# Kernel tuning notes

Hardware: AMD Instinct MI355X
Metric: run time of the kernel (lower is better)

## Reference

```python
import jax, jax.numpy as jnp
import numpy as np

N, E, G = 100000, 1600000, 8
IN, H, OUT = 3, 64, 20


def setup_inputs() -> dict:
    key = jax.random.key(0)
    ks = jax.random.split(key, 24)
    def nrm(k, shape, scale=0.1):
        return jax.random.normal(k, shape, dtype=jnp.float32) * scale
    inp = {}
    inp["x"] = jax.random.normal(ks[0], (N, IN), dtype=jnp.float32)
    inp["edge_index"] = jax.random.randint(ks[1], (2, E), 0, N, dtype=jnp.int32)
    inp["batch"] = jnp.sort(jax.random.randint(ks[2], (N,), 0, G, dtype=jnp.int32))
    dims = [(IN, H), (H, H), (H, H)]  # 3 GATConv layers (initial + layers-1)
    for i, (di, do) in enumerate(dims):
        inp[f"W{i}"] = nrm(ks[3 + 4 * i], (di, do))
        inp[f"as{i}"] = nrm(ks[4 + 4 * i], (do,))
        inp[f"ad{i}"] = nrm(ks[5 + 4 * i], (do,))
        inp[f"b{i}"] = jnp.zeros((do,), jnp.float32)
    inp["vn_emb0"] = jnp.zeros((1, H), jnp.float32)  # constant-0 init per module
    inp["m1_w1"] = nrm(ks[15], (H, H)); inp["m1_b1"] = jnp.zeros((H,), jnp.float32)
    inp["m1_w2"] = nrm(ks[16], (H, H)); inp["m1_b2"] = jnp.zeros((H,), jnp.float32)
    inp["mf_w1"] = nrm(ks[17], (H, H)); inp["mf_b1"] = jnp.zeros((H,), jnp.float32)
    inp["mf_w2"] = nrm(ks[18], (H, OUT)); inp["mf_b2"] = jnp.zeros((OUT,), jnp.float32)
    inp["out_w"] = nrm(ks[19], (H, OUT)); inp["out_b"] = jnp.zeros((OUT,), jnp.float32)
    return inp


def _gat(x, src, dst, W, a_s, a_d, b):
    # PyG GATConv, 1 head: h = xW; e_ij = LeakyReLU_0.2(a_s.h_j + a_d.h_i);
    # alpha = softmax over incoming edges of each dst node; out_i = sum_j alpha_ij h_j + b
    h = x @ W                                                  # [N, H]
    lg = jax.nn.leaky_relu((h @ a_s)[src] + (h @ a_d)[dst], 0.2)  # [E+N]
    m = jax.ops.segment_max(lg, dst, num_segments=N)
    m = jnp.where(jnp.isfinite(m), m, 0.0)
    p = jnp.exp(lg - m[dst])
    denom = jax.ops.segment_sum(p, dst, num_segments=N)
    alpha = p / denom[dst]
    return jax.ops.segment_sum(alpha[:, None] * h[src], dst, num_segments=N) + b


def _forward(x, edge_index, batch, params):
    (W0, as0, ad0, b0, W1, as1, ad1, b1, W2, as2, ad2, b2,
     vn_emb0, m1_w1, m1_b1, m1_w2, m1_b2, mf_w1, mf_b1, mf_w2, mf_b2,
     out_w, out_b) = params
    loops = jnp.arange(N, dtype=edge_index.dtype)  # GATConv add_self_loops=True
    src = jnp.concatenate([edge_index[0], loops])
    dst = jnp.concatenate([edge_index[1], loops])
    act = lambda v: jax.nn.leaky_relu(v, 0.01)  # nn.LeakyReLU default slope
    h = act(_gat(x, src, dst, W0, as0, ad0, b0))
    h = act(_gat(h, src, dst, W1, as1, ad1, b1))
    h = act(_gat(h, src, dst, W2, as2, ad2, b2))
    # virtual node: global_add_pool(out, batch) + Embedding(0) (zero-init)
    vn = jax.ops.segment_sum(h, batch, num_segments=G) + vn_emb0[0]
    vn = jax.nn.relu(vn @ m1_w1 + m1_b1)
    vn = jax.nn.relu(vn @ m1_w2 + m1_b2)
    vn = jax.nn.relu(vn @ mf_w1 + mf_b1)
    vn = jax.nn.relu(vn @ mf_w2 + mf_b2)
    return (h @ out_w + out_b, vn)


def reference(x, edge_index, batch, W0, as0, ad0, b0, W1, as1, ad1, b1,
              W2, as2, ad2, b2, vn_emb0, m1_w1, m1_b1, m1_w2, m1_b2,
              mf_w1, mf_b1, mf_w2, mf_b2, out_w, out_b):
    params = (W0, as0, ad0, b0, W1, as1, ad1, b1, W2, as2, ad2, b2,
              vn_emb0, m1_w1, m1_b1, m1_w2, m1_b2, mf_w1, mf_b1, mf_w2, mf_b2,
              out_w, out_b)
    return _forward(x, edge_index, batch, params)
```

## Files before the change

### kernel.cpp

```cpp
#include <hip/hip_runtime.h>
#include <hip/hip_bf16.h>

#define H 64
#define OUTD 20
#define NGRAPH 8
#define NBK 256
#define CAPB 8192
#define MAXDEG 63

typedef __attribute__((ext_vector_type(8))) short bf16x8;
typedef __attribute__((ext_vector_type(4))) float f32x4;
typedef __attribute__((ext_vector_type(8))) unsigned short u16x8;


__device__ __forceinline__ float ldp(const void* p, int i, bool f32) {
    return f32 ? ((const float*)p)[i]
               : __bfloat162float(((const __hip_bfloat16*)p)[i]);
}

__device__ __forceinline__ float bfu(unsigned short u) {
    union { unsigned int i; float f; } c; c.i = ((unsigned)u) << 16; return c.f;
}
__device__ __forceinline__ unsigned short fbits(float f) {
    __hip_bfloat16 b = __float2bfloat16(f);
    return *reinterpret_cast<unsigned short*>(&b);
}

__global__ void detect_dtype(const unsigned short* __restrict__ xb, int n_u16,
                             int* __restrict__ flag) {
    __shared__ int sh[256];
    int t = threadIdx.x;
    int m = min(n_u16, 4096);
    int bad = 0;
    for (int i = t; i < m; i += 256) {
        unsigned e = (xb[i] >> 7) & 0xFF;
        bad += (e >= 0x90) ? 1 : 0;
    }
    sh[t] = bad;
    __syncthreads();
    for (int off = 128; off; off >>= 1) {
        if (t < off) sh[t] += sh[t + off];
        __syncthreads();
    }
    if (t == 0) *flag = (sh[0] > (m >> 4)) ? 1 : 0;
}

__global__ void fillC_dense0(const int* __restrict__ src, const int* __restrict__ dst,
                             int* __restrict__ gcur, unsigned* __restrict__ ebuf,
                             int E, int n, int nC, int EPC, int nbk,
                             const void* __restrict__ x, const void* __restrict__ W,
                             const void* __restrict__ a_s, const void* __restrict__ a_d,
                             __hip_bfloat16* __restrict__ h, float* __restrict__ s,
                             float* __restrict__ d, const int* __restrict__ flagp) {
    if ((int)blockIdx.x < nC) {
        __shared__ unsigned lcnt[NBK];
        __shared__ int lbase[NBK];
        int t = threadIdx.x;
        for (int i = t; i < NBK; i += 256) lcnt[i] = 0;
        __syncthreads();
        int base = blockIdx.x * (256 * EPC) + t;
        for (int i = 0; i < EPC; ++i) {
            int e = base + i * 256;
            if (e < E) {
                int dn = dst[e];
                if ((unsigned)dn < (unsigned)n) atomicAdd(&lcnt[dn >> 9], 1u);
            }
        }
        __syncthreads();
        for (int i = t; i < nbk; i += 256) {
            unsigned c = lcnt[i];
            lbase[i] = c ? atomicAdd(&gcur[i], (int)c) : 0;
            lcnt[i] = 0;
        }
        __syncthreads();
        for (int i = 0; i < EPC; ++i) {
            int e = base + i * 256;
            if (e < E) {
                int dn = dst[e];
                if ((unsigned)dn < (unsigned)n) {
                    int b = dn >> 9;
                    unsigned pos = (unsigned)lbase[b] + atomicAdd(&lcnt[b], 1u);
                    if (pos < CAPB)
                        ebuf[(size_t)b * CAPB + pos] =
                            ((unsigned)src[e] << 9) | (unsigned)(dn & 511);
                }
            }
        }
        return;
    }
    const bool f32 = (*flagp != 0);
    int idx = ((int)blockIdx.x - nC) * 256 + threadIdx.x;
    int node = idx >> 6;
    int f = idx & 63;
    if (node >= n) return;
    float acc = 0.f;
    for (int k = 0; k < 3; ++k)
        acc += ldp(x, node * 3 + k, f32) * ldp(W, k * H + f, f32);
    ((short*)h)[((size_t)(f >> 3) * n + node) * 8 + (f & 7)] = (short)fbits(acc);
    float sv = acc * ldp(a_s, f, f32);
    float dv = acc * ldp(a_d, f, f32);
    for (int off = 32; off; off >>= 1) {
        sv += __shfl_xor(sv, off);
        dv += __shfl_xor(dv, off);
    }
    if (f == 0) { s[node] = sv; d[node] = dv; }
}

__global__ __launch_bounds__(512) void bucketD(const unsigned* __restrict__ ebuf,
                                               const int* __restrict__ gcur,
                                               unsigned* __restrict__ cntoff,
                                               unsigned* __restrict__ col,
                                               int* __restrict__ gtot, int n) {
    __shared__ unsigned lcnt[512];
    __shared__ int loff[512];
    __shared__ int sc[512];
    __shared__ int sdeg[512];
    __shared__ int sbase;
    int b = blockIdx.x, t = threadIdx.x;
    lcnt[t] = 0;
    __syncthreads();
    int end = min(gcur[b], CAPB);
    const unsigned* reg = ebuf + (size_t)b * CAPB;
    for (int i = t; i < end; i += 512) atomicAdd(&lcnt[reg[i] & 511u], 1u);
    __syncthreads();
    int node = (b << 9) + t;
    int degc = (node < n) ? (int)min(lcnt[t], (unsigned)MAXDEG) : -1;
    int slots = degc + 1;
    sc[t] = slots;
    __syncthreads();
    for (int ofs = 1; ofs < 512; ofs <<= 1) {
        int v = (t >= ofs) ? sc[t - ofs] : 0;
        __syncthreads();
        sc[t] += v;
        __syncthreads();
    }
    if (t == 511) sbase = atomicAdd(gtot, sc[511]);
    __syncthreads();
    int myoff = sbase + sc[t] - slots;
    int dg = (degc > 0) ? degc : 0;
    loff[t] = myoff;
    sdeg[t] = dg;
    if (node < n) cntoff[node] = (unsigned)myoff | ((unsigned)dg << 24);
    lcnt[t] = 0;
    __syncthreads();
    for (int i = t; i < end; i += 512) {
        unsigned e = reg[i];
        int loc = (int)(e & 511u);
        unsigned pos = atomicAdd(&lcnt[loc], 1u);
        if ((int)pos < sdeg[loc])
            col[loff[loc] + pos] = (e >> 9) << 15;
    }
}

__global__ void edge_weights(const float* __restrict__ s, const float* __restrict__ d,
                             const unsigned* __restrict__ cntoff,
                             unsigned* __restrict__ col, int n) {
    int node = ((int)blockIdx.x * 256 + (int)threadIdx.x) >> 4;
    if (node >= n) return;
    int l = threadIdx.x & 15;
    unsigned co = cntoff[node];
    int deg = (int)(co >> 24);
    int D = deg + 1;
    unsigned* cb = col + (co & 0xFFFFFFu);
    float di = d[node];
    int dm1 = D - 1;
    int e0 = l, e1 = l + 16, e2 = l + 32, e3 = l + 48;
    unsigned p0 = cb[min(e0, dm1)];
    unsigned p1 = cb[min(e1, dm1)];
    unsigned p2 = cb[min(e2, dm1)];
    unsigned p3 = cb[min(e3, dm1)];
    int j0 = (e0 < deg) ? (int)(p0 >> 15) : node;
    int j1 = (e1 < deg) ? (int)(p1 >> 15) : node;
    int j2 = (e2 < deg) ? (int)(p2 >> 15) : node;
    int j3 = (e3 < deg) ? (int)(p3 >> 15) : node;
    if ((unsigned)j0 >= (unsigned)n) j0 = 0;
    if ((unsigned)j1 >= (unsigned)n) j1 = 0;
    if ((unsigned)j2 >= (unsigned)n) j2 = 0;
    if ((unsigned)j3 >= (unsigned)n) j3 = 0;
    float v0 = s[j0] + di, v1 = s[j1] + di, v2 = s[j2] + di, v3 = s[j3] + di;
    v0 = v0 > 0.f ? v0 : 0.2f * v0;
    v1 = v1 > 0.f ? v1 : 0.2f * v1;
    v2 = v2 > 0.f ? v2 : 0.2f * v2;
    v3 = v3 > 0.f ? v3 : 0.2f * v3;
    bool m0 = e0 < D, m1 = e1 < D, m2 = e2 < D, m3 = e3 < D;
    float a0 = m0 ? v0 : -INFINITY, a1 = m1 ? v1 : -INFINITY;
    float a2 = m2 ? v2 : -INFINITY, a3 = m3 ? v3 : -INFINITY;
    float mx = fmaxf(fmaxf(a0, a1), fmaxf(a2, a3));
    for (int o = 1; o < 16; o <<= 1) mx = fmaxf(mx, __shfl_xor(mx, o));
    float x0 = m0 ? __expf(v0 - mx) : 0.f;
    float x1 = m1 ? __expf(v1 - mx) : 0.f;
    float x2 = m2 ? __expf(v2 - mx) : 0.f;
    float x3 = m3 ? __expf(v3 - mx) : 0.f;
    float ws = x0 + x1 + x2 + x3;
    for (int o = 1; o < 16; o <<= 1) ws += __shfl_xor(ws, o);
    float inv = 1.f / fmaxf(ws, 1e-20f);
    if (m0) cb[e0] = ((unsigned)j0 << 15) |
                     (((__float_as_uint(x0 * inv) + 0x8000u) >> 16) & 0x7FFFu);
    if (m1) cb[e1] = ((unsigned)j1 << 15) |
                     (((__float_as_uint(x1 * inv) + 0x8000u) >> 16) & 0x7FFFu);
    if (m2) cb[e2] = ((unsigned)j2 << 15) |
                     (((__float_as_uint(x2 * inv) + 0x8000u) >> 16) & 0x7FFFu);
    if (m3) cb[e3] = ((unsigned)j3 << 15) |
                     (((__float_as_uint(x3 * inv) + 0x8000u) >> 16) & 0x7FFFu);
}

#define ACC8(w, hv) { \
    a[0] += w * bfu(hv[0]); a[1] += w * bfu(hv[1]); \
    a[2] += w * bfu(hv[2]); a[3] += w * bfu(hv[3]); \
    a[4] += w * bfu(hv[4]); a[5] += w * bfu(hv[5]); \
    a[6] += w * bfu(hv[6]); a[7] += w * bfu(hv[7]); }

__global__ void gat_agg_sliced(const short* __restrict__ hs,
                               const unsigned* __restrict__ cntoff,
                               const unsigned* __restrict__ col,
                               const void* __restrict__ bias,
                               short* __restrict__ outs, int n, int halfN,
                               const int* __restrict__ flagp) {
    const bool f32 = (*flagp != 0);
    int shp = (int)blockIdx.x & 7;
    int sp = shp >> 1, half = shp & 1;
    int node = half * halfN + ((int)blockIdx.x >> 3) * 16 + ((int)threadIdx.x >> 4);
    int lim = half ? n : halfN;
    if (node >= lim) return;
    int l = threadIdx.x & 15;
    int c = l & 1, q = l >> 1;
    unsigned co = cntoff[node];
    int D = (int)(co >> 24) + 1;
    const unsigned* cb = col + (co & 0xFFFFFFu);
    int slice = 2 * sp + c;
    const u16x8* h8 = (const u16x8*)hs + (size_t)slice * n;

    int dm1 = D - 1;
    unsigned pk0 = cb[min(q, dm1)];
    unsigned pk1 = cb[min(q + 8, dm1)];
    unsigned pk2 = cb[min(q + 16, dm1)];
    unsigned pk3 = cb[min(q + 24, dm1)];
    unsigned pk4 = cb[min(q + 32, dm1)];
    unsigned pk5 = cb[min(q + 40, dm1)];
    unsigned pk6 = cb[min(q + 48, dm1)];
    unsigned pk7 = cb[min(q + 56, dm1)];
    pk0 = (q < D) ? pk0 : 0u;
    pk1 = (q + 8 < D) ? pk1 : 0u;
    pk2 = (q + 16 < D) ? pk2 : 0u;
    pk3 = (q + 24 < D) ? pk3 : 0u;
    pk4 = (q + 32 < D) ? pk4 : 0u;
    pk5 = (q + 40 < D) ? pk5 : 0u;
    pk6 = (q + 48 < D) ? pk6 : 0u;
    pk7 = (q + 56 < D) ? pk7 : 0u;

    float a[8] = {0.f, 0.f, 0.f, 0.f, 0.f, 0.f, 0.f, 0.f};
    {
        u16x8 hv0 = h8[pk0 >> 15];
        u16x8 hv1 = h8[pk1 >> 15];
        u16x8 hv2 = h8[pk2 >> 15];
        float w0 = __uint_as_float((pk0 & 0x7FFFu) << 16);
        float w1 = __uint_as_float((pk1 & 0x7FFFu) << 16);
        float w2 = __uint_as_float((pk2 & 0x7FFFu) << 16);
        ACC8(w0, hv0);
        ACC8(w1, hv1);
        ACC8(w2, hv2);
    }
    if (D > 24) {
        u16x8 hv3 = h8[pk3 >> 15];
        u16x8 hv4 = h8[pk4 >> 15];
        u16x8 hv5 = h8[pk5 >> 15];
        u16x8 hv6 = h8[pk6 >> 15];
        u16x8 hv7 = h8[pk7 >> 15];
        float w3 = __uint_as_float((pk3 & 0x7FFFu) << 16);
        float w4 = __uint_as_float((pk4 & 0x7FFFu) << 16);
        float w5 = __uint_as_float((pk5 & 0x7FFFu) << 16);
        float w6 = __uint_as_float((pk6 & 0x7FFFu) << 16);
        float w7 = __uint_as_float((pk7 & 0x7FFFu) << 16);
        ACC8(w3, hv3);
        ACC8(w4, hv4);
        ACC8(w5, hv5);
        ACC8(w6, hv6);
        ACC8(w7, hv7);
    }
#pragma unroll
    for (int i = 0; i < 8; ++i) {
        a[i] += __shfl_xor(a[i], 2);
        a[i] += __shfl_xor(a[i], 4);
        a[i] += __shfl_xor(a[i], 8);
    }
    if (q == 0) {
        u16x8 ov;
        for (int i = 0; i < 8; ++i) {
            float o = a[i] + ldp(bias, slice * 8 + i, f32);
            o = o > 0.f ? o : 0.01f * o;
            ov[i] = fbits(o);
        }
        *((u16x8*)outs + (size_t)slice * n + node) = ov;
    }
}


__global__ __launch_bounds__(256) void denseN_mfma(
    const __hip_bfloat16* __restrict__ in,
    const void* __restrict__ W,
    const void* __restrict__ a_s, const void* __restrict__ a_d,
    __hip_bfloat16* __restrict__ h, float* __restrict__ s,
    float* __restrict__ d, int n, const int* __restrict__ flagp) {
    const bool f32 = (*flagp != 0);
    __shared__ short Wt[64 * 72];
    int t = threadIdx.x;
    for (int i = t; i < 4096; i += 256) {
        int k = i >> 6, nf = i & 63;
        Wt[nf * 72 + k] = (short)fbits(ldp(W, i, f32));
    }
    __syncthreads();

    int wid = t >> 6, lane = t & 63;
    int quad = lane >> 4, n16 = lane & 15;
    int nodeBase = blockIdx.x * 64 + wid * 16;
    int mrow = nodeBase + n16;
    int mclamp = min(mrow, n - 1);
    const short* inp = (const short*)in;
    bf16x8 a0 = *(const bf16x8*)(inp + ((size_t)quad * n + mclamp) * 8);
    bf16x8 a1 = *(const bf16x8*)(inp + ((size_t)(4 + quad) * n + mclamp) * 8);

    float as_v[4], ad_v[4];
    for (int nt = 0; nt < 4; ++nt) {
        as_v[nt] = ldp(a_s, nt * 16 + n16, f32);
        ad_v[nt] = ldp(a_d, nt * 16 + n16, f32);
    }

    float sv[4] = {0.f, 0.f, 0.f, 0.f}, dv[4] = {0.f, 0.f, 0.f, 0.f};
    f32x4 accs[4];
    for (int nt = 0; nt < 4; ++nt) {
        const short* wrow = Wt + (nt * 16 + n16) * 72;
        bf16x8 b0 = *(const bf16x8*)(wrow + quad * 8);
        bf16x8 b1 = *(const bf16x8*)(wrow + 32 + quad * 8);
        f32x4 cacc = {0.f, 0.f, 0.f, 0.f};
        cacc = __builtin_amdgcn_mfma_f32_16x16x32_bf16(a0, b0, cacc, 0, 0, 0);
        cacc = __builtin_amdgcn_mfma_f32_16x16x32_bf16(a1, b1, cacc, 0, 0, 0);
        accs[nt] = cacc;
        for (int r = 0; r < 4; ++r) {
            sv[r] += cacc[r] * as_v[nt];
            dv[r] += cacc[r] * ad_v[nt];
        }
    }

    short* hb = (short*)h;
    for (int r = 0; r < 4; ++r) {
        int node = nodeBase + quad * 4 + r;
        if (node < n) {
            for (int nt = 0; nt < 4; ++nt) {
                int f = nt * 16 + n16;
                hb[((size_t)(f >> 3) * n + node) * 8 + (f & 7)] = (short)fbits(accs[nt][r]);
            }
        }
    }
    for (int r = 0; r < 4; ++r) {
        for (int mask = 1; mask < 16; mask <<= 1) {
            sv[r] += __shfl_xor(sv[r], mask);
            dv[r] += __shfl_xor(dv[r], mask);
        }
    }
    if (n16 == 0) {
        for (int r = 0; r < 4; ++r) {
            int node = nodeBase + quad * 4 + r;
            if (node < n) { s[node] = sv[r]; d[node] = dv[r]; }
        }
    }
}


__global__ __launch_bounds__(256) void proj_pool(
    const __hip_bfloat16* __restrict__ h,
    const void* __restrict__ W, const void* __restrict__ b,
    void* __restrict__ out, int n, const int* __restrict__ flagp,
    int projBlocks, const int* __restrict__ batch, float* __restrict__ vn) {
    const bool f32 = (*flagp != 0);
    if ((int)blockIdx.x < projBlocks) {
        __shared__ short Wt[32 * 72];
        int t = threadIdx.x;
        for (int i = t; i < 32 * 64; i += 256) {
            int o = i >> 6, k = i & 63;
            Wt[o * 72 + k] = (o < OUTD) ? (short)fbits(ldp(W, k * OUTD + o, f32)) : 0;
        }
        __syncthreads();

        int wid = t >> 6, lane = t & 63;
        int quad = lane >> 4, n16 = lane & 15;
        int nodeBase = blockIdx.x * 64 + wid * 16;
        int mclamp = min(nodeBase + n16, n - 1);
        const short* hsrc = (const short*)h;
        bf16x8 a0 = *(const bf16x8*)(hsrc + ((size_t)quad * n + mclamp) * 8);
        bf16x8 a1 = *(const bf16x8*)(hsrc + ((size_t)(4 + quad) * n + mclamp) * 8);

        f32x4 acc0 = {0.f, 0.f, 0.f, 0.f}, acc1 = {0.f, 0.f, 0.f, 0.f};
        {
            const short* wrow = Wt + n16 * 72;
            bf16x8 b0 = *(const bf16x8*)(wrow + quad * 8);
            bf16x8 b1 = *(const bf16x8*)(wrow + 32 + quad * 8);
            acc0 = __builtin_amdgcn_mfma_f32_16x16x32_bf16(a0, b0, acc0, 0, 0, 0);
            acc0 = __builtin_amdgcn_mfma_f32_16x16x32_bf16(a1, b1, acc0, 0, 0, 0);
        }
        {
            const short* wrow = Wt + (16 + n16) * 72;
            bf16x8 b0 = *(const bf16x8*)(wrow + quad * 8);
            bf16x8 b1 = *(const bf16x8*)(wrow + 32 + quad * 8);
            acc1 = __builtin_amdgcn_mfma_f32_16x16x32_bf16(a0, b0, acc1, 0, 0, 0);
            acc1 = __builtin_amdgcn_mfma_f32_16x16x32_bf16(a1, b1, acc1, 0, 0, 0);
        }
        float bv0 = ldp(b, n16, f32);
        float bv1 = (n16 < OUTD - 16) ? ldp(b, 16 + n16, f32) : 0.f;
        for (int r = 0; r < 4; ++r) {
            int node = nodeBase + quad * 4 + r;
            if (node >= n) break;
            float o0 = acc0[r] + bv0;
            if (f32) ((float*)out)[node * OUTD + n16] = o0;
            else     ((__hip_bfloat16*)out)[node * OUTD + n16] = __float2bfloat16(o0);
            if (n16 < OUTD - 16) {
                float o1 = acc1[r] + bv1;
                if (f32) ((float*)out)[node * OUTD + 16 + n16] = o1;
                else     ((__hip_bfloat16*)out)[node * OUTD + 16 + n16] = __float2bfloat16(o1);
            }
        }
        return;
    }
    __shared__ float part[NGRAPH * H];
    int t = threadIdx.x;
    for (int i = t; i < NGRAPH * H; i += 256) part[i] = 0.f;
    __syncthreads();
    int pb = (int)blockIdx.x - projBlocks;
    int npb = gridDim.x - projBlocks;
    int wid = t >> 6, lane = t & 63;
    int gwave = pb * 4 + wid;
    int nwaves = npb * 4;
    int chunk = (n + nwaves - 1) / nwaves;
    int beg = gwave * chunk;
    int end = min(n, beg + chunk);
    if (beg < end) {
        const short* hb = (const short*)h + (size_t)(lane >> 3) * n * 8 + (lane & 7);
        float acc = 0.f;
        int cur = batch[beg];
        for (int i = beg; i < end; ++i) {
            int g = batch[i];
            if (g != cur) {
                if ((unsigned)cur < NGRAPH) atomicAdd(&part[cur * H + lane], acc);
                acc = 0.f;
                cur = g;
            }
            acc += bfu((unsigned short)hb[(size_t)i * 8]);
        }
        if ((unsigned)cur < NGRAPH) atomicAdd(&part[cur * H + lane], acc);
    }
    __syncthreads();
    for (int i = t; i < NGRAPH * H; i += 256) {
        float v = part[i];
        if (v != 0.f) atomicAdd(&vn[i], v);
    }
}


__global__ void vn_mlp(const float* __restrict__ vn, const void* __restrict__ emb,
                       const void* __restrict__ w1, const void* __restrict__ b1,
                       const void* __restrict__ w2, const void* __restrict__ b2,
                       const void* __restrict__ w3, const void* __restrict__ b3,
                       const void* __restrict__ w4, const void* __restrict__ b4,
                       void* __restrict__ out, int out1_off, const int* __restrict__ flagp) {
    const bool f32 = (*flagp != 0);
    __shared__ float A[NGRAPH * H], B[NGRAPH * H];
    int t = threadIdx.x;
    int g = t >> 6, f = t & 63;
    A[t] = vn[t] + ldp(emb, f, f32);
    __syncthreads();
    float acc = ldp(b1, f, f32);
    for (int k = 0; k < H; ++k) acc += A[g * H + k] * ldp(w1, k * H + f, f32);
    B[t] = fmaxf(acc, 0.f);
    __syncthreads();
    acc = ldp(b2, f, f32);
    for (int k = 0; k < H; ++k) acc += B[g * H + k] * ldp(w2, k * H + f, f32);
    A[t] = fmaxf(acc, 0.f);
    __syncthreads();
    acc = ldp(b3, f, f32);
    for (int k = 0; k < H; ++k) acc += A[g * H + k] * ldp(w3, k * H + f, f32);
    B[t] = fmaxf(acc, 0.f);
    __syncthreads();
    if (f < OUTD) {
        acc = ldp(b4, f, f32);
        for (int k = 0; k < H; ++k) acc += B[g * H + k] * ldp(w4, k * OUTD + f, f32);
        acc = fmaxf(acc, 0.f);
        int idx = out1_off + g * OUTD + f;
        if (f32) ((float*)out)[idx] = acc;
        else     ((__hip_bfloat16*)out)[idx] = __float2bfloat16(acc);
    }
}


extern "C" void kernel_launch(void* const* d_in, const int* in_sizes, int n_in,
                              void* d_out, int out_size, void* d_ws, size_t ws_size,
                              hipStream_t stream) {
    const void* x   = d_in[0];
    const int* ei   = (const int*)d_in[1];
    const int* batch= (const int*)d_in[2];
    const void* W0  = d_in[3];
    const void* as0 = d_in[4];
    const void* ad0 = d_in[5];
    const void* b0  = d_in[6];
    const void* W1  = d_in[7];
    const void* as1 = d_in[8];
    const void* ad1 = d_in[9];
    const void* b1  = d_in[10];
    const void* W2  = d_in[11];
    const void* as2 = d_in[12];
    const void* ad2 = d_in[13];
    const void* b2  = d_in[14];
    const void* vne = d_in[15];
    const void* m1w1 = d_in[16];
    const void* m1b1 = d_in[17];
    const void* m1w2 = d_in[18];
    const void* m1b2 = d_in[19];
    const void* mfw1 = d_in[20];
    const void* mfb1 = d_in[21];
    const void* mfw2 = d_in[22];
    const void* mfb2 = d_in[23];
    const void* outw = d_in[24];
    const void* outb = d_in[25];

    const int N = in_sizes[2];
    const int E = in_sizes[1] / 2;
    const int* srcp = ei;
    const int* dstp = ei + E;

    char* w = (char*)d_ws;
    auto alloc = [&](size_t bytes) -> void* {
        void* p = (void*)w;
        w += ((bytes + 255) / 256) * 256;
        return p;
    };
    int*   flag   = (int*)alloc(256);
    int*   gcur   = (int*)alloc((size_t)NBK * 4);
    int*   gtot   = (int*)alloc(256);
    unsigned* ebuf= (unsigned*)alloc((size_t)NBK * CAPB * 4);
    unsigned* cntoff = (unsigned*)alloc((size_t)N * 4);
    unsigned* col = (unsigned*)alloc(((size_t)E + N + 64) * 4);
    __hip_bfloat16* featA = (__hip_bfloat16*)alloc((size_t)N * H * 2);
    __hip_bfloat16* featB = (__hip_bfloat16*)alloc((size_t)N * H * 2);
    __hip_bfloat16* hbuf  = (__hip_bfloat16*)alloc((size_t)N * H * 2);
    float* sArr   = (float*)alloc((size_t)N * 4);
    float* dArr   = (float*)alloc((size_t)N * 4);
    float* vn     = (float*)alloc((size_t)NGRAPH * H * 4);

    const int nbN64 = (N * H + 255) / 256;
    const int nb64 = (N + 63) / 64;
    const int projBlocks = (N + 63) / 64;
    const int nbk = (N + 511) >> 9;
    const int ewBlocks = (N + 15) / 16;
    const int halfN = (N + 1) / 2;
    const int aggBlocks = 8 * ((halfN + 15) / 16);
    int EPC = 32;
    int nC = (E + 256 * EPC - 1) / (256 * EPC);
    while (nC > 256) { EPC <<= 1; nC = (E + 256 * EPC - 1) / (256 * EPC); }

    detect_dtype<<<1, 256, 0, stream>>>((const unsigned short*)x, in_sizes[0], flag);

    hipMemsetAsync(gcur, 0, (size_t)NBK * 4, stream);
    hipMemsetAsync(gtot, 0, 4, stream);
    hipMemsetAsync(vn, 0, (size_t)NGRAPH * H * 4, stream);
    fillC_dense0<<<nC + nbN64, 256, 0, stream>>>(
        srcp, dstp, gcur, ebuf, E, N, nC, EPC, nbk,
        x, W0, as0, ad0, hbuf, sArr, dArr, flag);
    bucketD<<<nbk, 512, 0, stream>>>(ebuf, gcur, cntoff, col, gtot, N);

    edge_weights<<<ewBlocks, 256, 0, stream>>>(sArr, dArr, cntoff, col, N);
    gat_agg_sliced<<<aggBlocks, 256, 0, stream>>>((const short*)hbuf, cntoff, col,
                                                  b0, (short*)featA, N, halfN, flag);
    denseN_mfma<<<nb64, 256, 0, stream>>>(featA, W1, as1, ad1, hbuf, sArr, dArr, N, flag);
    edge_weights<<<ewBlocks, 256, 0, stream>>>(sArr, dArr, cntoff, col, N);
    gat_agg_sliced<<<aggBlocks, 256, 0, stream>>>((const short*)hbuf, cntoff, col,
                                                  b1, (short*)featB, N, halfN, flag);
    denseN_mfma<<<nb64, 256, 0, stream>>>(featB, W2, as2, ad2, hbuf, sArr, dArr, N, flag);
    edge_weights<<<ewBlocks, 256, 0, stream>>>(sArr, dArr, cntoff, col, N);
    gat_agg_sliced<<<aggBlocks, 256, 0, stream>>>((const short*)hbuf, cntoff, col,
                                                  b2, (short*)featA, N, halfN, flag);

    proj_pool<<<projBlocks + 512, 256, 0, stream>>>(featA, outw, outb, d_out, N, flag,
                                                    projBlocks, batch, vn);
    vn_mlp<<<1, 512, 0, stream>>>(vn, vne, m1w1, m1b1, m1w2, m1b2, mfw1, mfb1, mfw2, mfb2,
                                  d_out, N * OUTD, flag);
}
```

Before: 495.8 us.

## Use 32-feature slab layout, fuse first edge-weight pass into bucketing

Changes the bf16 feature layout from eight 8-wide slices to two 32-wide slabs per node. Aggregation now runs 32 lanes per node, so each gathered neighbour row is a contiguous 64-byte access split across 4 lanes, and the upper edge indices are loaded only when the degree exceeds 24. The layer-0 edge softmax weight computation is folded into the end of bucketD, removing one kernel launch and a reread of cntoff. All producers and consumers (dense kernels, pooling) are updated to the new indexing. Fewer nodes per block may affect occupancy and latency hiding.

```diff
diff --git a/kernel.cpp b/kernel.cpp
--- a/kernel.cpp
+++ b/kernel.cpp
@@ -45,125 +45,11 @@
     if (t == 0) *flag = (sh[0] > (m >> 4)) ? 1 : 0;
 }
 
-__global__ void fillC_dense0(const int* __restrict__ src, const int* __restrict__ dst,
-                             int* __restrict__ gcur, unsigned* __restrict__ ebuf,
-                             int E, int n, int nC, int EPC, int nbk,
-                             const void* __restrict__ x, const void* __restrict__ W,
-                             const void* __restrict__ a_s, const void* __restrict__ a_d,
-                             __hip_bfloat16* __restrict__ h, float* __restrict__ s,
-                             float* __restrict__ d, const int* __restrict__ flagp) {
-    if ((int)blockIdx.x < nC) {
-        __shared__ unsigned lcnt[NBK];
-        __shared__ int lbase[NBK];
-        int t = threadIdx.x;
-        for (int i = t; i < NBK; i += 256) lcnt[i] = 0;
-        __syncthreads();
-        int base = blockIdx.x * (256 * EPC) + t;
-        for (int i = 0; i < EPC; ++i) {
-            int e = base + i * 256;
-            if (e < E) {
-                int dn = dst[e];
-                if ((unsigned)dn < (unsigned)n) atomicAdd(&lcnt[dn >> 9], 1u);
-            }
-        }
-        __syncthreads();
-        for (int i = t; i < nbk; i += 256) {
-            unsigned c = lcnt[i];
-            lbase[i] = c ? atomicAdd(&gcur[i], (int)c) : 0;
-            lcnt[i] = 0;
-        }
-        __syncthreads();
-        for (int i = 0; i < EPC; ++i) {
-            int e = base + i * 256;
-            if (e < E) {
-                int dn = dst[e];
-                if ((unsigned)dn < (unsigned)n) {
-                    int b = dn >> 9;
-                    unsigned pos = (unsigned)lbase[b] + atomicAdd(&lcnt[b], 1u);
-                    if (pos < CAPB)
-                        ebuf[(size_t)b * CAPB + pos] =
-                            ((unsigned)src[e] << 9) | (unsigned)(dn & 511);
-                }
-            }
-        }
-        return;
-    }
-    const bool f32 = (*flagp != 0);
-    int idx = ((int)blockIdx.x - nC) * 256 + threadIdx.x;
-    int node = idx >> 6;
-    int f = idx & 63;
-    if (node >= n) return;
-    float acc = 0.f;
-    for (int k = 0; k < 3; ++k)
-        acc += ldp(x, node * 3 + k, f32) * ldp(W, k * H + f, f32);
-    ((short*)h)[((size_t)(f >> 3) * n + node) * 8 + (f & 7)] = (short)fbits(acc);
-    float sv = acc * ldp(a_s, f, f32);
-    float dv = acc * ldp(a_d, f, f32);
-    for (int off = 32; off; off >>= 1) {
-        sv += __shfl_xor(sv, off);
-        dv += __shfl_xor(dv, off);
-    }
-    if (f == 0) { s[node] = sv; d[node] = dv; }
-}
-
-__global__ __launch_bounds__(512) void bucketD(const unsigned* __restrict__ ebuf,
-                                               const int* __restrict__ gcur,
-                                               unsigned* __restrict__ cntoff,
-                                               unsigned* __restrict__ col,
-                                               int* __restrict__ gtot, int n) {
-    __shared__ unsigned lcnt[512];
-    __shared__ int loff[512];
-    __shared__ int sc[512];
-    __shared__ int sdeg[512];
-    __shared__ int sbase;
-    int b = blockIdx.x, t = threadIdx.x;
-    lcnt[t] = 0;
-    __syncthreads();
-    int end = min(gcur[b], CAPB);
-    const unsigned* reg = ebuf + (size_t)b * CAPB;
-    for (int i = t; i < end; i += 512) atomicAdd(&lcnt[reg[i] & 511u], 1u);
-    __syncthreads();
-    int node = (b << 9) + t;
-    int degc = (node < n) ? (int)min(lcnt[t], (unsigned)MAXDEG) : -1;
-    int slots = degc + 1;
-    sc[t] = slots;
-    __syncthreads();
-    for (int ofs = 1; ofs < 512; ofs <<= 1) {
-        int v = (t >= ofs) ? sc[t - ofs] : 0;
-        __syncthreads();
-        sc[t] += v;
-        __syncthreads();
-    }
-    if (t == 511) sbase = atomicAdd(gtot, sc[511]);
-    __syncthreads();
-    int myoff = sbase + sc[t] - slots;
-    int dg = (degc > 0) ? degc : 0;
-    loff[t] = myoff;
-    sdeg[t] = dg;
-    if (node < n) cntoff[node] = (unsigned)myoff | ((unsigned)dg << 24);
-    lcnt[t] = 0;
-    __syncthreads();
-    for (int i = t; i < end; i += 512) {
-        unsigned e = reg[i];
-        int loc = (int)(e & 511u);
-        unsigned pos = atomicAdd(&lcnt[loc], 1u);
-        if ((int)pos < sdeg[loc])
-            col[loff[loc] + pos] = (e >> 9) << 15;
-    }
-}
-
-__global__ void edge_weights(const float* __restrict__ s, const float* __restrict__ d,
-                             const unsigned* __restrict__ cntoff,
-                             unsigned* __restrict__ col, int n) {
-    int node = ((int)blockIdx.x * 256 + (int)threadIdx.x) >> 4;
-    if (node >= n) return;
-    int l = threadIdx.x & 15;
-    unsigned co = cntoff[node];
-    int deg = (int)(co >> 24);
+__device__ __forceinline__ void ew_node(const float* __restrict__ s, float di,
+                                        unsigned* __restrict__ cb,
+                                        int deg, int node, int n, int l) {
     int D = deg + 1;
-    unsigned* cb = col + (co & 0xFFFFFFu);
-    float di = d[node];
-    int dm1 = D - 1;
+    int dm1 = deg;
     int e0 = l, e1 = l + 16, e2 = l + 32, e3 = l + 48;
     unsigned p0 = cb[min(e0, dm1)];
     unsigned p1 = cb[min(e1, dm1)];
@@ -204,6 +90,134 @@
                      (((__float_as_uint(x3 * inv) + 0x8000u) >> 16) & 0x7FFFu);
 }
 
+__global__ void fillC_dense0(const int* __restrict__ src, const int* __restrict__ dst,
+                             int* __restrict__ gcur, unsigned* __restrict__ ebuf,
+                             int E, int n, int nC, int EPC, int nbk,
+                             const void* __restrict__ x, const void* __restrict__ W,
+                             const void* __restrict__ a_s, const void* __restrict__ a_d,
+                             __hip_bfloat16* __restrict__ h, float* __restrict__ s,
+                             float* __restrict__ d, const int* __restrict__ flagp) {
+    if ((int)blockIdx.x < nC) {
+        __shared__ unsigned lcnt[NBK];
+        __shared__ int lbase[NBK];
+        int t = threadIdx.x;
+        for (int i = t; i < NBK; i += 256) lcnt[i] = 0;
+        __syncthreads();
+        int base = blockIdx.x * (256 * EPC) + t;
+        for (int i = 0; i < EPC; ++i) {
+            int e = base + i * 256;
+            if (e < E) {
+                int dn = dst[e];
+                if ((unsigned)dn < (unsigned)n) atomicAdd(&lcnt[dn >> 9], 1u);
+            }
+        }
+        __syncthreads();
+        for (int i = t; i < nbk; i += 256) {
+            unsigned c = lcnt[i];
+            lbase[i] = c ? atomicAdd(&gcur[i], (int)c) : 0;
+            lcnt[i] = 0;
+        }
+        __syncthreads();
+        for (int i = 0; i < EPC; ++i) {
+            int e = base + i * 256;
+            if (e < E) {
+                int dn = dst[e];
+                if ((unsigned)dn < (unsigned)n) {
+                    int b = dn >> 9;
+                    unsigned pos = (unsigned)lbase[b] + atomicAdd(&lcnt[b], 1u);
+                    if (pos < CAPB)
+                        ebuf[(size_t)b * CAPB + pos] =
+                            ((unsigned)src[e] << 9) | (unsigned)(dn & 511);
+                }
+            }
+        }
+        return;
+    }
+    const bool f32 = (*flagp != 0);
+    int idx = ((int)blockIdx.x - nC) * 256 + threadIdx.x;
+    int node = idx >> 6;
+    int f = idx & 63;
+    if (node >= n) return;
+    float acc = 0.f;
+    for (int k = 0; k < 3; ++k)
+        acc += ldp(x, node * 3 + k, f32) * ldp(W, k * H + f, f32);
+    ((short*)h)[((size_t)(f >> 5) * n + node) * 32 + (f & 31)] = (short)fbits(acc);
+    float sv = acc * ldp(a_s, f, f32);
+    float dv = acc * ldp(a_d, f, f32);
+    for (int off = 32; off; off >>= 1) {
+        sv += __shfl_xor(sv, off);
+        dv += __shfl_xor(dv, off);
+    }
+    if (f == 0) { s[node] = sv; d[node] = dv; }
+}
+
+__global__ __launch_bounds__(512) void bucketD(const unsigned* __restrict__ ebuf,
+                                               const int* __restrict__ gcur,
+                                               unsigned* __restrict__ cntoff,
+                                               unsigned* __restrict__ col,
+                                               int* __restrict__ gtot, int n,
+                                               const float* __restrict__ s,
+                                               const float* __restrict__ d) {
+    __shared__ unsigned lcnt[512];
+    __shared__ int loff[512];
+    __shared__ int sc[512];
+    __shared__ int sdeg[512];
+    __shared__ int sbase;
+    int b = blockIdx.x, t = threadIdx.x;
+    lcnt[t] = 0;
+    __syncthreads();
+    int end = min(gcur[b], CAPB);
+    const unsigned* reg = ebuf + (size_t)b * CAPB;
+    for (int i = t; i < end; i += 512) atomicAdd(&lcnt[reg[i] & 511u], 1u);
+    __syncthreads();
+    int node = (b << 9) + t;
+    int degc = (node < n) ? (int)min(lcnt[t], (unsigned)MAXDEG) : -1;
+    int slots = degc + 1;
+    sc[t] = slots;
+    __syncthreads();
+    for (int ofs = 1; ofs < 512; ofs <<= 1) {
+        int v = (t >= ofs) ? sc[t - ofs] : 0;
+        __syncthreads();
+        sc[t] += v;
+        __syncthreads();
+    }
+    if (t == 511) sbase = atomicAdd(gtot, sc[511]);
+    __syncthreads();
+    int myoff = sbase + sc[t] - slots;
+    int dg = (degc > 0) ? degc : 0;
+    loff[t] = myoff;
+    sdeg[t] = dg;
+    if (node < n) cntoff[node] = (unsigned)myoff | ((unsigned)dg << 24);
+    lcnt[t] = 0;
+    __syncthreads();
+    for (int i = t; i < end; i += 512) {
+        unsigned e = reg[i];
+        int loc = (int)(e & 511u);
+        unsigned pos = atomicAdd(&lcnt[loc], 1u);
+        if ((int)pos < sdeg[loc])
+            col[loff[loc] + pos] = (e >> 9) << 15;
+    }
+    __syncthreads();
+    int l = t & 15;
+    int base16 = t >> 4;
+    for (int it = 0; it < 16; ++it) {
+        int local = base16 + 32 * it;
+        int nd = (b << 9) + local;
+        if (nd < n)
+            ew_node(s, d[nd], col + loff[local], sdeg[local], nd, n, l);
+    }
+}
+
+__global__ void edge_weights(const float* __restrict__ s, const float* __restrict__ d,
+                             const unsigned* __restrict__ cntoff,
+                             unsigned* __restrict__ col, int n) {
+    int node = ((int)blockIdx.x * 256 + (int)threadIdx.x) >> 4;
+    if (node >= n) return;
+    unsigned co = cntoff[node];
+    ew_node(s, d[node], col + (co & 0xFFFFFFu), (int)(co >> 24), node, n,
+            threadIdx.x & 15);
+}
+
 #define ACC8(w, hv) { \
     a[0] += w * bfu(hv[0]); a[1] += w * bfu(hv[1]); \
     a[2] += w * bfu(hv[2]); a[3] += w * bfu(hv[3]); \
@@ -214,45 +228,35 @@
                                const unsigned* __restrict__ cntoff,
                                const unsigned* __restrict__ col,
                                const void* __restrict__ bias,
-                               short* __restrict__ outs, int n, int halfN,
+                               short* __restrict__ outs, int n,
                                const int* __restrict__ flagp) {
     const bool f32 = (*flagp != 0);
     int shp = (int)blockIdx.x & 7;
-    int sp = shp >> 1, half = shp & 1;
-    int node = half * halfN + ((int)blockIdx.x >> 3) * 16 + ((int)threadIdx.x >> 4);
-    int lim = half ? n : halfN;
+    int fh = shp >> 2, nq = shp & 3;
+    int qN = (n + 3) >> 2;
+    int node = nq * qN + ((int)blockIdx.x >> 3) * 8 + ((int)threadIdx.x >> 5);
+    int lim = min(n, (nq + 1) * qN);
     if (node >= lim) return;
-    int l = threadIdx.x & 15;
-    int c = l & 1, q = l >> 1;
+    int l = threadIdx.x & 31;
+    int c = l & 3, q = l >> 2;
     unsigned co = cntoff[node];
     int D = (int)(co >> 24) + 1;
     const unsigned* cb = col + (co & 0xFFFFFFu);
-    int slice = 2 * sp + c;
-    const u16x8* h8 = (const u16x8*)hs + (size_t)slice * n;
+    const u16x8* h8 = (const u16x8*)hs + (size_t)fh * n * 4 + c;
 
     int dm1 = D - 1;
     unsigned pk0 = cb[min(q, dm1)];
     unsigned pk1 = cb[min(q + 8, dm1)];
     unsigned pk2 = cb[min(q + 16, dm1)];
-    unsigned pk3 = cb[min(q + 24, dm1)];
-    unsigned pk4 = cb[min(q + 32, dm1)];
-    unsigned pk5 = cb[min(q + 40, dm1)];
-    unsigned pk6 = cb[min(q + 48, dm1)];
-    unsigned pk7 = cb[min(q + 56, dm1)];
     pk0 = (q < D) ? pk0 : 0u;
     pk1 = (q + 8 < D) ? pk1 : 0u;
     pk2 = (q + 16 < D) ? pk2 : 0u;
-    pk3 = (q + 24 < D) ? pk3 : 0u;
-    pk4 = (q + 32 < D) ? pk4 : 0u;
-    pk5 = (q + 40 < D) ? pk5 : 0u;
-    pk6 = (q + 48 < D) ? pk6 : 0u;
-    pk7 = (q + 56 < D) ? pk7 : 0u;
 
     float a[8] = {0.f, 0.f, 0.f, 0.f, 0.f, 0.f, 0.f, 0.f};
     {
-        u16x8 hv0 = h8[pk0 >> 15];
-        u16x8 hv1 = h8[pk1 >> 15];
-        u16x8 hv2 = h8[pk2 >> 15];
+        u16x8 hv0 = h8[(size_t)(pk0 >> 15) * 4];
+        u16x8 hv1 = h8[(size_t)(pk1 >> 15) * 4];
+        u16x8 hv2 = h8[(size_t)(pk2 >> 15) * 4];
         float w0 = __uint_as_float((pk0 & 0x7FFFu) << 16);
         float w1 = __uint_as_float((pk1 & 0x7FFFu) << 16);
         float w2 = __uint_as_float((pk2 & 0x7FFFu) << 16);
@@ -261,11 +265,21 @@
         ACC8(w2, hv2);
     }
     if (D > 24) {
-        u16x8 hv3 = h8[pk3 >> 15];
-        u16x8 hv4 = h8[pk4 >> 15];
-        u16x8 hv5 = h8[pk5 >> 15];
-        u16x8 hv6 = h8[pk6 >> 15];
-        u16x8 hv7 = h8[pk7 >> 15];
+        unsigned pk3 = cb[min(q + 24, dm1)];
+        unsigned pk4 = cb[min(q + 32, dm1)];
+        unsigned pk5 = cb[min(q + 40, dm1)];
+        unsigned pk6 = cb[min(q + 48, dm1)];
+        unsigned pk7 = cb[min(q + 56, dm1)];
+        pk3 = (q + 24 < D) ? pk3 : 0u;
+        pk4 = (q + 32 < D) ? pk4 : 0u;
+        pk5 = (q + 40 < D) ? pk5 : 0u;
+        pk6 = (q + 48 < D) ? pk6 : 0u;
+        pk7 = (q + 56 < D) ? pk7 : 0u;
+        u16x8 hv3 = h8[(size_t)(pk3 >> 15) * 4];
+        u16x8 hv4 = h8[(size_t)(pk4 >> 15) * 4];
+        u16x8 hv5 = h8[(size_t)(pk5 >> 15) * 4];
+        u16x8 hv6 = h8[(size_t)(pk6 >> 15) * 4];
+        u16x8 hv7 = h8[(size_t)(pk7 >> 15) * 4];
         float w3 = __uint_as_float((pk3 & 0x7FFFu) << 16);
         float w4 = __uint_as_float((pk4 & 0x7FFFu) << 16);
         float w5 = __uint_as_float((pk5 & 0x7FFFu) << 16);
@@ -279,18 +293,18 @@
     }
 #pragma unroll
     for (int i = 0; i < 8; ++i) {
-        a[i] += __shfl_xor(a[i], 2);
         a[i] += __shfl_xor(a[i], 4);
         a[i] += __shfl_xor(a[i], 8);
+        a[i] += __shfl_xor(a[i], 16);
     }
     if (q == 0) {
         u16x8 ov;
         for (int i = 0; i < 8; ++i) {
-            float o = a[i] + ldp(bias, slice * 8 + i, f32);
+            float o = a[i] + ldp(bias, fh * 32 + c * 8 + i, f32);
             o = o > 0.f ? o : 0.01f * o;
             ov[i] = fbits(o);
         }
-        *((u16x8*)outs + (size_t)slice * n + node) = ov;
+        ((u16x8*)outs)[((size_t)fh * n + node) * 4 + c] = ov;
     }
 }
 
@@ -316,8 +330,8 @@
     int mrow = nodeBase + n16;
     int mclamp = min(mrow, n - 1);
     const short* inp = (const short*)in;
-    bf16x8 a0 = *(const bf16x8*)(inp + ((size_t)quad * n + mclamp) * 8);
-    bf16x8 a1 = *(const bf16x8*)(inp + ((size_t)(4 + quad) * n + mclamp) * 8);
+    bf16x8 a0 = *(const bf16x8*)(inp + (size_t)mclamp * 32 + quad * 8);
+    bf16x8 a1 = *(const bf16x8*)(inp + ((size_t)n + mclamp) * 32 + quad * 8);
 
     float as_v[4], ad_v[4];
     for (int nt = 0; nt < 4; ++nt) {
@@ -347,7 +361,7 @@
         if (node < n) {
             for (int nt = 0; nt < 4; ++nt) {
                 int f = nt * 16 + n16;
-                hb[((size_t)(f >> 3) * n + node) * 8 + (f & 7)] = (short)fbits(accs[nt][r]);
+                hb[((size_t)(f >> 5) * n + node) * 32 + (f & 31)] = (short)fbits(accs[nt][r]);
             }
         }
     }
@@ -386,8 +400,8 @@
         int nodeBase = blockIdx.x * 64 + wid * 16;
         int mclamp = min(nodeBase + n16, n - 1);
         const short* hsrc = (const short*)h;
-        bf16x8 a0 = *(const bf16x8*)(hsrc + ((size_t)quad * n + mclamp) * 8);
-        bf16x8 a1 = *(const bf16x8*)(hsrc + ((size_t)(4 + quad) * n + mclamp) * 8);
+        bf16x8 a0 = *(const bf16x8*)(hsrc + (size_t)mclamp * 32 + quad * 8);
+        bf16x8 a1 = *(const bf16x8*)(hsrc + ((size_t)n + mclamp) * 32 + quad * 8);
 
         f32x4 acc0 = {0.f, 0.f, 0.f, 0.f}, acc1 = {0.f, 0.f, 0.f, 0.f};
         {
@@ -433,7 +447,7 @@
     int beg = gwave * chunk;
     int end = min(n, beg + chunk);
     if (beg < end) {
-        const short* hb = (const short*)h + (size_t)(lane >> 3) * n * 8 + (lane & 7);
+        const short* hb = (const short*)h + (size_t)(lane >> 5) * n * 32 + (lane & 31);
         float acc = 0.f;
         int cur = batch[beg];
         for (int i = beg; i < end; ++i) {
@@ -443,7 +457,7 @@
                 acc = 0.f;
                 cur = g;
             }
-            acc += bfu((unsigned short)hb[(size_t)i * 8]);
+            acc += bfu((unsigned short)hb[(size_t)i * 32]);
         }
         if ((unsigned)cur < NGRAPH) atomicAdd(&part[cur * H + lane], acc);
     }
@@ -549,8 +563,8 @@
     const int projBlocks = (N + 63) / 64;
     const int nbk = (N + 511) >> 9;
     const int ewBlocks = (N + 15) / 16;
-    const int halfN = (N + 1) / 2;
-    const int aggBlocks = 8 * ((halfN + 15) / 16);
+    const int qN = (N + 3) >> 2;
+    const int aggBlocks = 8 * ((qN + 7) / 8);
     int EPC = 32;
     int nC = (E + 256 * EPC - 1) / (256 * EPC);
     while (nC > 256) { EPC <<= 1; nC = (E + 256 * EPC - 1) / (256 * EPC); }
@@ -563,19 +577,18 @@
     fillC_dense0<<<nC + nbN64, 256, 0, stream>>>(
         srcp, dstp, gcur, ebuf, E, N, nC, EPC, nbk,
         x, W0, as0, ad0, hbuf, sArr, dArr, flag);
-    bucketD<<<nbk, 512, 0, stream>>>(ebuf, gcur, cntoff, col, gtot, N);
-
-    edge_weights<<<ewBlocks, 256, 0, stream>>>(sArr, dArr, cntoff, col, N);
+    bucketD<<<nbk, 512, 0, stream>>>(ebuf, gcur, cntoff, col, gtot, N, sArr, dArr);
+
     gat_agg_sliced<<<aggBlocks, 256, 0, stream>>>((const short*)hbuf, cntoff, col,
-                                                  b0, (short*)featA, N, halfN, flag);
+                                                  b0, (short*)featA, N, flag);
     denseN_mfma<<<nb64, 256, 0, stream>>>(featA, W1, as1, ad1, hbuf, sArr, dArr, N, flag);
     edge_weights<<<ewBlocks, 256, 0, stream>>>(sArr, dArr, cntoff, col, N);
     gat_agg_sliced<<<aggBlocks, 256, 0, stream>>>((const short*)hbuf, cntoff, col,
-                                                  b1, (short*)featB, N, halfN, flag);
+                                                  b1, (short*)featB, N, flag);
     denseN_mfma<<<nb64, 256, 0, stream>>>(featB, W2, as2, ad2, hbuf, sArr, dArr, N, flag);
     edge_weights<<<ewBlocks, 256, 0, stream>>>(sArr, dArr, cntoff, col, N);
     gat_agg_sliced<<<aggBlocks, 256, 0, stream>>>((const short*)hbuf, cntoff, col,
-                                                  b2, (short*)featA, N, halfN, flag);
+                                                  b2, (short*)featA, N, flag);
 
     proj_pool<<<projBlocks + 512, 256, 0, stream>>>(featA, outw, outb, d_out, N, flag,
                                                     projBlocks, batch, vn);
```

After: 422.9 us. 14.7% less time.
